# Kernel tuning notes

Measured on AMD Instinct MI355X. Metric: run time of the kernel, lower is better.

## Reference

```python
import jax, jax.numpy as jnp
import numpy as np

B, T, D = 8, 1024, 1024
H = 16
ATT_DIM = 1024
VAL_DIM = 1024
SCALE = float((D // H) ** 0.5)  # note: uses input_dim//num_heads, not head dim of attention_dim
EPS = 1e-13


def setup_inputs() -> dict:
    key = jax.random.key(0)
    ks = jax.random.split(key, 6)
    inputs = jax.random.normal(ks[0], (B, T, D), dtype=jnp.float32)
    mask = jnp.ones((B, T), dtype=jnp.float32)
    adj = jax.random.uniform(ks[1], (B, T, T), dtype=jnp.float32)
    # combined QKV projection: Linear(D, 2*ATT_DIM + VAL_DIM)
    W_qkv = jax.random.normal(ks[2], (2 * ATT_DIM + VAL_DIM, D), dtype=jnp.float32) * (1.0 / np.sqrt(D))
    b_qkv = jnp.zeros((2 * ATT_DIM + VAL_DIM,), dtype=jnp.float32)
    # output projection: Linear(VAL_DIM, D)
    W_out = jax.random.normal(ks[3], (D, VAL_DIM), dtype=jnp.float32) * (1.0 / np.sqrt(VAL_DIM))
    b_out = jnp.zeros((D,), dtype=jnp.float32)
    return {"inputs": inputs, "mask": mask, "adj": adj,
            "W_qkv": W_qkv, "b_qkv": b_qkv, "W_out": W_out, "b_out": b_out}


def reference(inputs, mask, adj, W_qkv, b_qkv, W_out, b_out):
    b, t, _ = inputs.shape
    dh_a = ATT_DIM // H
    dh_v = VAL_DIM // H
    proj = jnp.einsum('btd,od->bto', inputs, W_qkv) + b_qkv
    q = proj[..., :ATT_DIM]
    k = proj[..., ATT_DIM:2 * ATT_DIM]
    v = proj[..., 2 * ATT_DIM:]
    # [B, H, T, dh]
    q = q.reshape(b, t, H, dh_a).transpose(0, 2, 1, 3)
    k = k.reshape(b, t, H, dh_a).transpose(0, 2, 1, 3)
    v = v.reshape(b, t, H, dh_v).transpose(0, 2, 1, 3)
    scores = jnp.einsum('bhqd,bhkd->bhqk', q, k) / SCALE
    # multiplicative adjacency gate, broadcast over heads
    scores = scores * adj[:, None, :, :]
    # old-allennlp masked_softmax: softmax(scores * mask), re-mask, renormalize
    m = mask[:, None, None, :]  # [B,1,1,T]
    attn = jax.nn.softmax(scores * m, axis=-1)
    attn = attn * m
    attn = attn / (attn.sum(axis=-1, keepdims=True) + EPS)
    out = jnp.einsum('bhqk,bhkd->bhqd', attn, v)  # [B,H,T,dh_v]
    out = out.transpose(0, 2, 1, 3).reshape(b, t, VAL_DIM)
    out = jnp.einsum('btv,ov->bto', out, W_out) + b_out
    return out
```

## Files before the change

kernel.cpp:

```cpp
#include <hip/hip_runtime.h>
#include <hip/hip_bf16.h>
#include <cstdint>


using bf16 = __hip_bfloat16;
typedef __attribute__((ext_vector_type(8))) short short8;
typedef __attribute__((ext_vector_type(4))) short short4v;
typedef __attribute__((ext_vector_type(4))) float floatx4;
typedef __attribute__((ext_vector_type(2))) unsigned int uint2v;

#define B_    8
#define T_    1024
#define D_    1024
#define H_    16
#define PROJW 3072

__device__ __forceinline__ void gl2lds16(const void* g, void* l) {
  __builtin_amdgcn_global_load_lds(
      (const __attribute__((address_space(1))) void*)g,
      (__attribute__((address_space(3))) void*)l,
      16, 0, 0);
}

__device__ __forceinline__ unsigned short f2b_bits(float f) {
  return __builtin_bit_cast(unsigned short, __float2bfloat16(f));
}

__device__ __forceinline__ float fast_exp2(float x) {
#if __has_builtin(__builtin_amdgcn_exp2f)
  return __builtin_amdgcn_exp2f(x);
#else
  float r;
  asm("v_exp_f32 %0, %1\ns_nop 0" : "=v"(r) : "v"(x));
  return r;
#endif
}

__device__ __forceinline__ void cvt_quad(const float* s, bf16* d, int i) {
  floatx4 f = *(const floatx4*)(s + i);
  short4v h;
  h[0] = f2b_bits(f[0]); h[1] = f2b_bits(f[1]);
  h[2] = f2b_bits(f[2]); h[3] = f2b_bits(f[3]);
  *(short4v*)(d + i) = h;
}

__global__ __launch_bounds__(256)
void cvt2_f32_bf16(const float* __restrict__ sa, bf16* __restrict__ da, int nq_a,
                   const float* __restrict__ sb, bf16* __restrict__ db) {
  int q = blockIdx.x * 256 + threadIdx.x;
  if (q < nq_a) cvt_quad(sa, da, q * 4);
  else          cvt_quad(sb, db, (q - nq_a) * 4);
}

template<int EPI>
__global__ __launch_bounds__(512)
void gemm_bt_bias(const bf16* __restrict__ A, const bf16* __restrict__ Bm,
                  const float* __restrict__ bias, void* __restrict__ C0,
                  void* __restrict__ C1, void* __restrict__ C2,
                  int M, int N, int K)
{
  __shared__ __align__(16) unsigned short sA[2][128 * 64];
  __shared__ __align__(16) unsigned short sB[2][128 * 64];

  const int tid  = threadIdx.x;
  const int lane = tid & 63;
  const int wv   = tid >> 6;
  const int quad = lane >> 4;
  const int l16  = lane & 15;
  const int wm   = wv >> 1;
  const int wn   = wv & 1;

  const int gx   = gridDim.x;
  const int nwg  = gx * gridDim.y;
  const int bidl = blockIdx.y * gx + blockIdx.x;
  const int xcd  = bidl & 7;
  const int c    = bidl >> 3;
  const int cpx  = nwg >> 3;
  const int R    = cpx / gx;
  const int nb   = c / (R * 4);
  const int rem  = c % (R * 4);
  const int bm   = xcd * R + (rem >> 2);
  const int bn   = nb * 4 + (rem & 3);

  floatx4 acc[2][4];
#pragma unroll
  for (int i = 0; i < 2; ++i)
#pragma unroll
    for (int j = 0; j < 4; ++j) acc[i][j] = (floatx4){0.f, 0.f, 0.f, 0.f};

  const int o_base = wv * 1024 + lane * 16;
  const bf16* gA[2];
  const bf16* gB[2];
#pragma unroll
  for (int it = 0; it < 2; ++it) {
    int o   = it * 8192 + o_base;
    int row = o >> 7;
    int col = ((o & 127) ^ ((row & 7) << 4)) >> 1;
    gA[it] = A  + (size_t)(bm * 128 + row) * K + col;
    gB[it] = Bm + (size_t)(bn * 128 + row) * K + col;
  }

  const int NT = K >> 6;
#pragma unroll
  for (int it = 0; it < 2; ++it)
    gl2lds16(gA[it], &sA[0][(it * 8192 + wv * 1024) >> 1]);
#pragma unroll
  for (int it = 0; it < 2; ++it)
    gl2lds16(gB[it], &sB[0][(it * 8192 + wv * 1024) >> 1]);

  const int swx = (l16 & 7) << 3;

  for (int t = 0; t < NT; ++t) {
    const int s = t & 1;
    if (t + 1 < NT) {
#pragma unroll
      for (int it = 0; it < 2; ++it)
        gl2lds16(gA[it] + (size_t)(t + 1) * 64, &sA[s ^ 1][(it * 8192 + wv * 1024) >> 1]);
#pragma unroll
      for (int it = 0; it < 2; ++it)
        gl2lds16(gB[it] + (size_t)(t + 1) * 64, &sB[s ^ 1][(it * 8192 + wv * 1024) >> 1]);
      __builtin_amdgcn_sched_barrier(0);
      asm volatile("s_waitcnt vmcnt(4)" ::: "memory");
    } else {
      asm volatile("s_waitcnt vmcnt(0)" ::: "memory");
    }
    __builtin_amdgcn_s_barrier();
    __builtin_amdgcn_sched_barrier(0);

#pragma unroll
    for (int kk = 0; kk < 64; kk += 32) {
      short8 a_[2], b_[4];
#pragma unroll
      for (int i = 0; i < 2; ++i)
        a_[i] = *(const short8*)&sA[s][(wm * 32 + i * 16 + l16) * 64 + ((kk + quad * 8) ^ swx)];
#pragma unroll
      for (int j = 0; j < 4; ++j)
        b_[j] = *(const short8*)&sB[s][(wn * 64 + j * 16 + l16) * 64 + ((kk + quad * 8) ^ swx)];
#pragma unroll
      for (int i = 0; i < 2; ++i)
#pragma unroll
        for (int j = 0; j < 4; ++j)
          acc[i][j] = __builtin_amdgcn_mfma_f32_16x16x32_bf16(a_[i], b_[j], acc[i][j], 0, 0, 0);
    }

    __builtin_amdgcn_sched_barrier(0);
    __builtin_amdgcn_s_barrier();
  }

  {
    const int region = bn >> 3;
    if (region < 2) {
      bf16* dst = (bf16*)(region == 0 ? C0 : C1);
#pragma unroll
      for (int j = 0; j < 4; ++j) {
        const int colg = bn * 128 + wn * 64 + j * 16 + l16;
        const int colr = colg & 1023;
        const float bv = bias[colg];
#pragma unroll
        for (int i = 0; i < 2; ++i)
#pragma unroll
          for (int r = 0; r < 4; ++r) {
            int rowg = bm * 128 + wm * 32 + i * 16 + quad * 4 + r;
            dst[(size_t)rowg * 1024 + colr] = __float2bfloat16(acc[i][j][r] + bv);
          }
      }
    } else {
      bf16* vt = (bf16*)C2;
#pragma unroll
      for (int j = 0; j < 4; ++j) {
        const int colg = bn * 128 + wn * 64 + j * 16 + l16;
        const int d  = colg & 63;
        const int hh = (colg >> 6) & 15;
        const float bv = bias[colg];
#pragma unroll
        for (int i = 0; i < 2; ++i) {
          int rowg0 = bm * 128 + wm * 32 + i * 16 + quad * 4;
          int bb = rowg0 >> 10, t0 = rowg0 & 1023;
          short4v pk;
#pragma unroll
          for (int r = 0; r < 4; ++r) pk[r] = (short)f2b_bits(acc[i][j][r] + bv);
          *(short4v*)&vt[((size_t)(bb * 16 + hh) << 16) + ((size_t)d << 10) + t0] = pk;
        }
      }
    }
  }
}

__global__ __launch_bounds__(512)
void gemm_out_f32b(const bf16* __restrict__ A, const float* __restrict__ Bw,
                   const float* __restrict__ bias, float* __restrict__ C0,
                   int M, int N, int K)
{
  __shared__ __align__(16) unsigned short sA[2][128 * 64];
  __shared__ __align__(16) unsigned short sB[2][128 * 64];

  const int tid  = threadIdx.x;
  const int lane = tid & 63;
  const int wv   = tid >> 6;
  const int quad = lane >> 4;
  const int l16  = lane & 15;
  const int wm   = wv >> 1;
  const int wn   = wv & 1;

  const int gx   = gridDim.x;
  const int nwg  = gx * gridDim.y;
  const int bidl = blockIdx.y * gx + blockIdx.x;
  const int xcd  = bidl & 7;
  const int c    = bidl >> 3;
  const int cpx  = nwg >> 3;
  const int R    = cpx / gx;
  const int nb   = c / (R * 4);
  const int rem  = c % (R * 4);
  const int bm   = xcd * R + (rem >> 2);
  const int bn   = nb * 4 + (rem & 3);

  floatx4 acc[2][4];
#pragma unroll
  for (int i = 0; i < 2; ++i)
#pragma unroll
    for (int j = 0; j < 4; ++j) acc[i][j] = (floatx4){0.f, 0.f, 0.f, 0.f};

  const int o_base = wv * 1024 + lane * 16;
  const bf16*  gA[2];
  const float* gBf[2];
  int ldsOff[2];
#pragma unroll
  for (int it = 0; it < 2; ++it) {
    int o   = it * 8192 + o_base;
    int row = o >> 7;
    int col = ((o & 127) ^ ((row & 7) << 4)) >> 1;
    gA[it]  = A  + (size_t)(bm * 128 + row) * K + col;
    gBf[it] = Bw + (size_t)(bn * 128 + row) * K + col;
    ldsOff[it] = ((it * 8192 + wv * 1024) >> 1) + lane * 8;
  }

  const int NT = K >> 6;

  {
    floatx4 q0a = *(const floatx4*)(gBf[0]);
    floatx4 q0b = *(const floatx4*)(gBf[0] + 4);
    floatx4 q1a = *(const floatx4*)(gBf[1]);
    floatx4 q1b = *(const floatx4*)(gBf[1] + 4);
#pragma unroll
    for (int it = 0; it < 2; ++it)
      gl2lds16(gA[it], &sA[0][(it * 8192 + wv * 1024) >> 1]);
    short8 h0, h1;
#pragma unroll
    for (int k = 0; k < 4; ++k) {
      h0[k] = f2b_bits(q0a[k]); h0[k + 4] = f2b_bits(q0b[k]);
      h1[k] = f2b_bits(q1a[k]); h1[k + 4] = f2b_bits(q1b[k]);
    }
    *(short8*)&sB[0][ldsOff[0]] = h0;
    *(short8*)&sB[0][ldsOff[1]] = h1;
    asm volatile("s_waitcnt lgkmcnt(0)" ::: "memory");
  }

  const int swx = (l16 & 7) << 3;

  for (int t = 0; t < NT; ++t) {
    const int s = t & 1;
    floatx4 q0a, q0b, q1a, q1b;
    if (t + 1 < NT) {
      q0a = *(const floatx4*)(gBf[0] + (size_t)(t + 1) * 64);
      q0b = *(const floatx4*)(gBf[0] + (size_t)(t + 1) * 64 + 4);
      q1a = *(const floatx4*)(gBf[1] + (size_t)(t + 1) * 64);
      q1b = *(const floatx4*)(gBf[1] + (size_t)(t + 1) * 64 + 4);
#pragma unroll
      for (int it = 0; it < 2; ++it)
        gl2lds16(gA[it] + (size_t)(t + 1) * 64, &sA[s ^ 1][(it * 8192 + wv * 1024) >> 1]);
      __builtin_amdgcn_sched_barrier(0);
      asm volatile("s_waitcnt vmcnt(6)" ::: "memory");
    } else {
      asm volatile("s_waitcnt vmcnt(0)" ::: "memory");
    }
    __builtin_amdgcn_s_barrier();
    __builtin_amdgcn_sched_barrier(0);

#pragma unroll
    for (int kk = 0; kk < 64; kk += 32) {
      short8 a_[2], b_[4];
#pragma unroll
      for (int i = 0; i < 2; ++i)
        a_[i] = *(const short8*)&sA[s][(wm * 32 + i * 16 + l16) * 64 + ((kk + quad * 8) ^ swx)];
#pragma unroll
      for (int j = 0; j < 4; ++j)
        b_[j] = *(const short8*)&sB[s][(wn * 64 + j * 16 + l16) * 64 + ((kk + quad * 8) ^ swx)];
#pragma unroll
      for (int i = 0; i < 2; ++i)
#pragma unroll
        for (int j = 0; j < 4; ++j)
          acc[i][j] = __builtin_amdgcn_mfma_f32_16x16x32_bf16(a_[i], b_[j], acc[i][j], 0, 0, 0);
    }

    __builtin_amdgcn_sched_barrier(0);
    if (t + 1 < NT) {
      asm volatile("s_waitcnt vmcnt(2)" ::: "memory");
      short8 h0, h1;
#pragma unroll
      for (int k = 0; k < 4; ++k) {
        h0[k] = f2b_bits(q0a[k]); h0[k + 4] = f2b_bits(q0b[k]);
        h1[k] = f2b_bits(q1a[k]); h1[k + 4] = f2b_bits(q1b[k]);
      }
      *(short8*)&sB[s ^ 1][ldsOff[0]] = h0;
      *(short8*)&sB[s ^ 1][ldsOff[1]] = h1;
      asm volatile("s_waitcnt lgkmcnt(0)" ::: "memory");
    }
    __builtin_amdgcn_sched_barrier(0);
    __builtin_amdgcn_s_barrier();
  }

#pragma unroll
  for (int j = 0; j < 4; ++j) {
    const int colg = bn * 128 + wn * 64 + j * 16 + l16;
    const float bv = bias[colg];
#pragma unroll
    for (int i = 0; i < 2; ++i)
#pragma unroll
      for (int r = 0; r < 4; ++r) {
        int rowg = bm * 128 + wm * 32 + i * 16 + quad * 4 + r;
        C0[(size_t)rowg * N + colg] = acc[i][j][r] + bv;
      }
  }
}

__global__ __launch_bounds__(512)
void attn_fused(const bf16* __restrict__ Qp, const bf16* __restrict__ Kp,
                const bf16* __restrict__ Vt, const float* __restrict__ adj,
                const float* __restrict__ mask, bf16* __restrict__ aout)
{
  __shared__ __align__(16) unsigned short sK[64 * 72];
  __shared__ __align__(16) unsigned short sVT[64 * 72];
  __shared__ __align__(16) unsigned short sP[128 * 72];

  const int tid  = threadIdx.x;
  const int lane = tid & 63;
  const int wv   = tid >> 6;
  const int quad = lane >> 4;
  const int l16  = lane & 15;

  const int bid  = blockIdx.x + 16 * (blockIdx.y + 8 * blockIdx.z);
  const int b    = bid & 7;
  const int slot = bid >> 3;
  const int h    = slot & 15;
  const int qt   = slot >> 4;

  const bf16* qbase = Qp + (size_t)(b * T_ + qt * 128 + wv * 16 + l16) * 1024 + h * 64 + quad * 8;
  const short8 aq0 = *(const short8*)qbase;
  const short8 aq1 = *(const short8*)(qbase + 32);

  const int srow  = tid >> 3;
  const int chunk = (tid & 7) * 8;
  const int sig = ((srow & 15) << 2) | (srow >> 4);
  const bf16* kb = Kp + (size_t)(b * T_ + sig) * 1024 + h * 64 + chunk;
  const bf16* vb = Vt + ((size_t)(b * 16 + h) << 16) + ((size_t)srow << 10) + chunk;

  const float* mb = mask + b * T_ + l16 * 4;
  const float* adjr[4];
#pragma unroll
  for (int r = 0; r < 4; ++r)
    adjr[r] = adj + ((size_t)b * T_ + qt * 128 + wv * 16 + quad * 4 + r) * T_ + l16 * 4;

  short8 kr = *(const short8*)kb;
  short8 vr = *(const short8*)vb;

  short8 ones8;
#pragma unroll
  for (int i = 0; i < 8; ++i) ones8[i] = (short)0x3F80;

  floatx4 oacc[4];
#pragma unroll
  for (int d = 0; d < 4; ++d) oacc[d] = (floatx4){0.f, 0.f, 0.f, 0.f};
  floatx4 Lacc = (floatx4){0.f, 0.f, 0.f, 0.f};

  const float SC = 0.125f * 1.44269504088896f;

  for (int kt = 0; kt < 16; ++kt) {
    floatx4 av[4];
    floatx4 mk4 = *(const floatx4*)(mb + kt * 64);
#pragma unroll
    for (int r = 0; r < 4; ++r) av[r] = *(const floatx4*)(adjr[r] + kt * 64);
    floatx4 cjv, offv;
#pragma unroll
    for (int j = 0; j < 4; ++j) {
      cjv[j]  = mk4[j] * SC;
      offv[j] = (mk4[j] == 0.f) ? -1e30f : 0.f;
    }

    __syncthreads();
    *(short8*)&sK [srow * 72 + chunk] = kr;
    *(short8*)&sVT[srow * 72 + chunk] = vr;
    __syncthreads();

    {
      int nk = kt < 15 ? kt + 1 : 15;
      kr = *(const short8*)(kb + ((size_t)nk << 16));
      vr = *(const short8*)(vb + (nk << 6));
    }

    floatx4 sacc[4];
#pragma unroll
    for (int j = 0; j < 4; ++j) sacc[j] = (floatx4){0.f, 0.f, 0.f, 0.f};
    __builtin_amdgcn_s_setprio(1);
#pragma unroll
    for (int kk = 0; kk < 64; kk += 32) {
      short8 aq = kk ? aq1 : aq0;
#pragma unroll
      for (int j = 0; j < 4; ++j) {
        short8 bk = *(const short8*)&sK[(j * 16 + l16) * 72 + kk + quad * 8];
        sacc[j] = __builtin_amdgcn_mfma_f32_16x16x32_bf16(aq, bk, sacc[j], 0, 0, 0);
      }
    }
    __builtin_amdgcn_s_setprio(0);

#pragma unroll
    for (int r = 0; r < 4; ++r) {
      floatx4 avc = av[r] * cjv;
      float p[4];
#pragma unroll
      for (int j = 0; j < 4; ++j) {
        float z = fminf(fmaf(sacc[j][r], avc[j], offv[j]), 100.f);
        p[j] = fast_exp2(z);
      }
      unsigned w0, w1;
      asm("v_cvt_pk_bf16_f32 %0, %1, %2" : "=v"(w0) : "v"(p[0]), "v"(p[1]));
      asm("v_cvt_pk_bf16_f32 %0, %1, %2" : "=v"(w1) : "v"(p[2]), "v"(p[3]));
      uint2v pw; pw[0] = w0; pw[1] = w1;
      *(uint2v*)&sP[(wv * 16 + quad * 4 + r) * 72 + l16 * 4] = pw;
    }

    __asm__ __volatile__("" ::: "memory");

    __builtin_amdgcn_s_setprio(1);
#pragma unroll
    for (int kk = 0; kk < 64; kk += 32) {
      short8 ap = *(const short8*)&sP[(wv * 16 + l16) * 72 + kk + quad * 8];
      Lacc = __builtin_amdgcn_mfma_f32_16x16x32_bf16(ap, ones8, Lacc, 0, 0, 0);
#pragma unroll
      for (int d = 0; d < 4; ++d) {
        short8 bv = *(const short8*)&sVT[(d * 16 + l16) * 72 + kk + quad * 8];
        oacc[d] = __builtin_amdgcn_mfma_f32_16x16x32_bf16(ap, bv, oacc[d], 0, 0, 0);
      }
    }
    __builtin_amdgcn_s_setprio(0);
  }

#pragma unroll
  for (int d = 0; d < 4; ++d) {
#pragma unroll
    for (int r = 0; r < 4; ++r) {
      int qrow = qt * 128 + wv * 16 + quad * 4 + r;
      float val = oacc[d][r] / (Lacc[r] + 1e-13f);
      aout[(size_t)(b * T_ + qrow) * 1024 + h * 64 + d * 16 + l16] = __float2bfloat16(val);
    }
  }
}

extern "C" void kernel_launch(void* const* d_in, const int* in_sizes, int n_in,
                              void* d_out, int out_size, void* d_ws, size_t ws_size,
                              hipStream_t stream) {
  const float* inputs = (const float*)d_in[0];
  const float* mask   = (const float*)d_in[1];
  const float* adj    = (const float*)d_in[2];
  const float* W_qkv  = (const float*)d_in[3];
  const float* b_qkv  = (const float*)d_in[4];
  const float* W_out  = (const float*)d_in[5];
  const float* b_out  = (const float*)d_in[6];

  const size_t SEG = (size_t)8192 * 1024;
  bf16* Qp   = (bf16*)d_ws;
  bf16* Kp   = Qp + SEG;
  bf16* Vt   = Kp + SEG;
  bf16* aout = Vt + SEG;

  bf16* ib_bf = (bf16*)d_out;
  bf16* wq_bf = ib_bf + SEG;

  dim3 blk(256);
  cvt2_f32_bf16<<<dim3((8192 * 1024 + 3072 * 1024) / 4 / 256), blk, 0, stream>>>(
      inputs, ib_bf, 8192 * 1024 / 4, W_qkv, wq_bf);
  gemm_bt_bias<2><<<dim3(PROJW / 128, (B_ * T_) / 128), dim3(512), 0, stream>>>(
      ib_bf, wq_bf, b_qkv, Qp, Kp, Vt, B_ * T_, PROJW, D_);
  attn_fused<<<dim3(H_, T_ / 128, B_), dim3(512), 0, stream>>>(Qp, Kp, Vt, adj, mask, aout);
  gemm_out_f32b<<<dim3(D_ / 128, (B_ * T_) / 128), dim3(512), 0, stream>>>(
      aout, W_out, b_out, (float*)d_out, B_ * T_, D_, D_);
}
```

Measured before the change: 267.2 us.

## Fuse fp32-to-bf16 conversion into QKV GEMM tile loads

Removes the standalone conversion kernel and has the QKV projection GEMM read fp32 inputs and weights directly, converting them to bf16 in registers before writing to LDS. This avoids writing and re-reading a bf16 copy of the inputs and weights and saves a kernel launch. In exchange, the GEMM now reads twice the bytes per tile (fp32), loses the async global-to-LDS path, and waits for vmcnt(0) after the MFMA block, which may expose load latency. The input and each weight tile are also converted repeatedly by every workgroup that loads them.

```diff
diff --git a/kernel.cpp b/kernel.cpp
--- a/kernel.cpp
+++ b/kernel.cpp
@@ -24,6 +24,15 @@
 
 __device__ __forceinline__ unsigned short f2b_bits(float f) {
   return __builtin_bit_cast(unsigned short, __float2bfloat16(f));
+}
+
+__device__ __forceinline__ short8 pack8(floatx4 a, floatx4 b) {
+  short8 h;
+  h[0] = f2b_bits(a[0]); h[1] = f2b_bits(a[1]);
+  h[2] = f2b_bits(a[2]); h[3] = f2b_bits(a[3]);
+  h[4] = f2b_bits(b[0]); h[5] = f2b_bits(b[1]);
+  h[6] = f2b_bits(b[2]); h[7] = f2b_bits(b[3]);
+  return h;
 }
 
 __device__ __forceinline__ float fast_exp2(float x) {
@@ -36,27 +45,10 @@
 #endif
 }
 
-__device__ __forceinline__ void cvt_quad(const float* s, bf16* d, int i) {
-  floatx4 f = *(const floatx4*)(s + i);
-  short4v h;
-  h[0] = f2b_bits(f[0]); h[1] = f2b_bits(f[1]);
-  h[2] = f2b_bits(f[2]); h[3] = f2b_bits(f[3]);
-  *(short4v*)(d + i) = h;
-}
-
-__global__ __launch_bounds__(256)
-void cvt2_f32_bf16(const float* __restrict__ sa, bf16* __restrict__ da, int nq_a,
-                   const float* __restrict__ sb, bf16* __restrict__ db) {
-  int q = blockIdx.x * 256 + threadIdx.x;
-  if (q < nq_a) cvt_quad(sa, da, q * 4);
-  else          cvt_quad(sb, db, (q - nq_a) * 4);
-}
-
-template<int EPI>
 __global__ __launch_bounds__(512)
-void gemm_bt_bias(const bf16* __restrict__ A, const bf16* __restrict__ Bm,
-                  const float* __restrict__ bias, void* __restrict__ C0,
-                  void* __restrict__ C1, void* __restrict__ C2,
+void gemm_qkv_f32(const float* __restrict__ A, const float* __restrict__ Bw,
+                  const float* __restrict__ bias, bf16* __restrict__ Qp,
+                  bf16* __restrict__ Kp, bf16* __restrict__ Vt,
                   int M, int N, int K)
 {
   __shared__ __align__(16) unsigned short sA[2][128 * 64];
@@ -89,42 +81,54 @@
     for (int j = 0; j < 4; ++j) acc[i][j] = (floatx4){0.f, 0.f, 0.f, 0.f};
 
   const int o_base = wv * 1024 + lane * 16;
-  const bf16* gA[2];
-  const bf16* gB[2];
+  const float* gAf[2];
+  const float* gBf[2];
+  int ldsOff[2];
 #pragma unroll
   for (int it = 0; it < 2; ++it) {
     int o   = it * 8192 + o_base;
     int row = o >> 7;
     int col = ((o & 127) ^ ((row & 7) << 4)) >> 1;
-    gA[it] = A  + (size_t)(bm * 128 + row) * K + col;
-    gB[it] = Bm + (size_t)(bn * 128 + row) * K + col;
+    gAf[it] = A  + (size_t)(bm * 128 + row) * K + col;
+    gBf[it] = Bw + (size_t)(bn * 128 + row) * K + col;
+    ldsOff[it] = ((it * 8192 + wv * 1024) >> 1) + lane * 8;
   }
 
   const int NT = K >> 6;
-#pragma unroll
-  for (int it = 0; it < 2; ++it)
-    gl2lds16(gA[it], &sA[0][(it * 8192 + wv * 1024) >> 1]);
-#pragma unroll
-  for (int it = 0; it < 2; ++it)
-    gl2lds16(gB[it], &sB[0][(it * 8192 + wv * 1024) >> 1]);
+
+  {
+    floatx4 a0a = *(const floatx4*)(gAf[0]);
+    floatx4 a0b = *(const floatx4*)(gAf[0] + 4);
+    floatx4 a1a = *(const floatx4*)(gAf[1]);
+    floatx4 a1b = *(const floatx4*)(gAf[1] + 4);
+    floatx4 b0a = *(const floatx4*)(gBf[0]);
+    floatx4 b0b = *(const floatx4*)(gBf[0] + 4);
+    floatx4 b1a = *(const floatx4*)(gBf[1]);
+    floatx4 b1b = *(const floatx4*)(gBf[1] + 4);
+    *(short8*)&sA[0][ldsOff[0]] = pack8(a0a, a0b);
+    *(short8*)&sA[0][ldsOff[1]] = pack8(a1a, a1b);
+    *(short8*)&sB[0][ldsOff[0]] = pack8(b0a, b0b);
+    *(short8*)&sB[0][ldsOff[1]] = pack8(b1a, b1b);
+    asm volatile("s_waitcnt lgkmcnt(0)" ::: "memory");
+    __builtin_amdgcn_s_barrier();
+  }
 
   const int swx = (l16 & 7) << 3;
 
   for (int t = 0; t < NT; ++t) {
     const int s = t & 1;
+    floatx4 a0a, a0b, a1a, a1b, b0a, b0b, b1a, b1b;
     if (t + 1 < NT) {
-#pragma unroll
-      for (int it = 0; it < 2; ++it)
-        gl2lds16(gA[it] + (size_t)(t + 1) * 64, &sA[s ^ 1][(it * 8192 + wv * 1024) >> 1]);
-#pragma unroll
-      for (int it = 0; it < 2; ++it)
-        gl2lds16(gB[it] + (size_t)(t + 1) * 64, &sB[s ^ 1][(it * 8192 + wv * 1024) >> 1]);
-      __builtin_amdgcn_sched_barrier(0);
-      asm volatile("s_waitcnt vmcnt(4)" ::: "memory");
-    } else {
-      asm volatile("s_waitcnt vmcnt(0)" ::: "memory");
-    }
-    __builtin_amdgcn_s_barrier();
+      const size_t ko = (size_t)(t + 1) * 64;
+      a0a = *(const floatx4*)(gAf[0] + ko);
+      a0b = *(const floatx4*)(gAf[0] + ko + 4);
+      a1a = *(const floatx4*)(gAf[1] + ko);
+      a1b = *(const floatx4*)(gAf[1] + ko + 4);
+      b0a = *(const floatx4*)(gBf[0] + ko);
+      b0b = *(const floatx4*)(gBf[0] + ko + 4);
+      b1a = *(const floatx4*)(gBf[1] + ko);
+      b1b = *(const floatx4*)(gBf[1] + ko + 4);
+    }
     __builtin_amdgcn_sched_barrier(0);
 
 #pragma unroll
@@ -143,6 +147,15 @@
           acc[i][j] = __builtin_amdgcn_mfma_f32_16x16x32_bf16(a_[i], b_[j], acc[i][j], 0, 0, 0);
     }
 
+    __builtin_amdgcn_sched_barrier(0);
+    if (t + 1 < NT) {
+      asm volatile("s_waitcnt vmcnt(0)" ::: "memory");
+      *(short8*)&sA[s ^ 1][ldsOff[0]] = pack8(a0a, a0b);
+      *(short8*)&sA[s ^ 1][ldsOff[1]] = pack8(a1a, a1b);
+      *(short8*)&sB[s ^ 1][ldsOff[0]] = pack8(b0a, b0b);
+      *(short8*)&sB[s ^ 1][ldsOff[1]] = pack8(b1a, b1b);
+      asm volatile("s_waitcnt lgkmcnt(0)" ::: "memory");
+    }
     __builtin_amdgcn_sched_barrier(0);
     __builtin_amdgcn_s_barrier();
   }
@@ -150,7 +163,7 @@
   {
     const int region = bn >> 3;
     if (region < 2) {
-      bf16* dst = (bf16*)(region == 0 ? C0 : C1);
+      bf16* dst = region == 0 ? Qp : Kp;
 #pragma unroll
       for (int j = 0; j < 4; ++j) {
         const int colg = bn * 128 + wn * 64 + j * 16 + l16;
@@ -165,7 +178,6 @@
           }
       }
     } else {
-      bf16* vt = (bf16*)C2;
 #pragma unroll
       for (int j = 0; j < 4; ++j) {
         const int colg = bn * 128 + wn * 64 + j * 16 + l16;
@@ -179,7 +191,7 @@
           short4v pk;
 #pragma unroll
           for (int r = 0; r < 4; ++r) pk[r] = (short)f2b_bits(acc[i][j][r] + bv);
-          *(short4v*)&vt[((size_t)(bb * 16 + hh) << 16) + ((size_t)d << 10) + t0] = pk;
+          *(short4v*)&Vt[((size_t)(bb * 16 + hh) << 16) + ((size_t)d << 10) + t0] = pk;
         }
       }
     }
@@ -244,14 +256,8 @@
 #pragma unroll
     for (int it = 0; it < 2; ++it)
       gl2lds16(gA[it], &sA[0][(it * 8192 + wv * 1024) >> 1]);
-    short8 h0, h1;
-#pragma unroll
-    for (int k = 0; k < 4; ++k) {
-      h0[k] = f2b_bits(q0a[k]); h0[k + 4] = f2b_bits(q0b[k]);
-      h1[k] = f2b_bits(q1a[k]); h1[k + 4] = f2b_bits(q1b[k]);
-    }
-    *(short8*)&sB[0][ldsOff[0]] = h0;
-    *(short8*)&sB[0][ldsOff[1]] = h1;
+    *(short8*)&sB[0][ldsOff[0]] = pack8(q0a, q0b);
+    *(short8*)&sB[0][ldsOff[1]] = pack8(q1a, q1b);
     asm volatile("s_waitcnt lgkmcnt(0)" ::: "memory");
   }
 
@@ -295,14 +301,8 @@
     __builtin_amdgcn_sched_barrier(0);
     if (t + 1 < NT) {
       asm volatile("s_waitcnt vmcnt(2)" ::: "memory");
-      short8 h0, h1;
-#pragma unroll
-      for (int k = 0; k < 4; ++k) {
-        h0[k] = f2b_bits(q0a[k]); h0[k + 4] = f2b_bits(q0b[k]);
-        h1[k] = f2b_bits(q1a[k]); h1[k + 4] = f2b_bits(q1b[k]);
-      }
-      *(short8*)&sB[s ^ 1][ldsOff[0]] = h0;
-      *(short8*)&sB[s ^ 1][ldsOff[1]] = h1;
+      *(short8*)&sB[s ^ 1][ldsOff[0]] = pack8(q0a, q0b);
+      *(short8*)&sB[s ^ 1][ldsOff[1]] = pack8(q1a, q1b);
       asm volatile("s_waitcnt lgkmcnt(0)" ::: "memory");
     }
     __builtin_amdgcn_sched_barrier(0);
@@ -472,14 +472,8 @@
   bf16* Vt   = Kp + SEG;
   bf16* aout = Vt + SEG;
 
-  bf16* ib_bf = (bf16*)d_out;
-  bf16* wq_bf = ib_bf + SEG;
-
-  dim3 blk(256);
-  cvt2_f32_bf16<<<dim3((8192 * 1024 + 3072 * 1024) / 4 / 256), blk, 0, stream>>>(
-      inputs, ib_bf, 8192 * 1024 / 4, W_qkv, wq_bf);
-  gemm_bt_bias<2><<<dim3(PROJW / 128, (B_ * T_) / 128), dim3(512), 0, stream>>>(
-      ib_bf, wq_bf, b_qkv, Qp, Kp, Vt, B_ * T_, PROJW, D_);
+  gemm_qkv_f32<<<dim3(PROJW / 128, (B_ * T_) / 128), dim3(512), 0, stream>>>(
+      inputs, W_qkv, b_qkv, Qp, Kp, Vt, B_ * T_, PROJW, D_);
   attn_fused<<<dim3(H_, T_ / 128, B_), dim3(512), 0, stream>>>(Qp, Kp, Vt, adj, mask, aout);
   gemm_out_f32b<<<dim3(D_ / 128, (B_ * T_) / 128), dim3(512), 0, stream>>>(
       aout, W_out, b_out, (float*)d_out, B_ * T_, D_, D_);
```

After: 301.0 us. 12.6% more time.
